# Kernel optimization log

Hardware: AMD Instinct MI355X
Metric: run time of the kernel (lower is better)

## Reference

```python
import jax, jax.numpy as jnp
import numpy as np

EPS = 0.3  # residual scaling from init_kwargs
N, E = 50000, 800000
IN_DIM, HID, OUT = 256, 64, 40


def setup_inputs() -> dict:
    key = jax.random.key(0)
    ks = jax.random.split(key, 8)
    h = jax.random.normal(ks[0], (N, IN_DIM), dtype=jnp.float32)
    src = jax.random.randint(ks[1], (E,), 0, N, dtype=jnp.int32)
    dst = jax.random.randint(ks[2], (E,), 0, N, dtype=jnp.int32)
    t1_w = jax.random.normal(ks[3], (HID, IN_DIM), dtype=jnp.float32) * 0.05
    t1_b = jnp.zeros((HID,), jnp.float32)
    gate_w1 = jax.random.normal(ks[4], (2 * HID,), dtype=jnp.float32) * 0.1
    gate_b1 = jnp.zeros((1,), jnp.float32)
    gate_w2 = jax.random.normal(ks[5], (2 * HID,), dtype=jnp.float32) * 0.1
    gate_b2 = jnp.zeros((1,), jnp.float32)
    t2_w = jax.random.normal(ks[6], (OUT, HID), dtype=jnp.float32) * 0.05
    t2_b = jnp.zeros((OUT,), jnp.float32)
    return {"h": h, "src": src, "dst": dst, "t1_w": t1_w, "t1_b": t1_b,
            "gate_w1": gate_w1, "gate_b1": gate_b1,
            "gate_w2": gate_w2, "gate_b2": gate_b2,
            "t2_w": t2_w, "t2_b": t2_b}


def _fa_layer(x, src, dst, d, gate_w, gate_b):
    # gate over concat([h_dst, h_src]) == h_dst @ w[:H] + h_src @ w[H:]
    H = x.shape[1]
    g = jnp.tanh(x[dst] @ gate_w[:H] + x[src] @ gate_w[H:] + gate_b[0])  # [E]
    e = g * d[dst] * d[src]                                              # [E]
    # message: u_mul_e('h','e') then sum onto dst
    z = jnp.zeros_like(x).at[dst].add(x[src] * e[:, None])               # [N,H]
    return z


def reference(h, src, dst, t1_w, t1_b, gate_w1, gate_b1, gate_w2, gate_b2, t2_w, t2_b):
    n = h.shape[0]
    # degree normalization d = deg^{-1/2} (in-degree, clamped to >=1)
    deg = jnp.zeros((n,), h.dtype).at[dst].add(jnp.ones_like(dst, h.dtype))
    d = jax.lax.rsqrt(jnp.maximum(deg, 1.0))
    # dropout is identity in eval mode
    x = jax.nn.relu(h @ t1_w.T + t1_b)
    raw = x
    for gw, gb in ((gate_w1, gate_b1), (gate_w2, gate_b2)):
        x = EPS * raw + _fa_layer(x, src, dst, d, gw, gb)
    logits = x @ t2_w.T + t2_b
    return jax.nn.log_softmax(logits, axis=1)
```

## Files before the change

### kernel.cpp

```cpp
#include <hip/hip_runtime.h>
#include <hip/hip_bf16.h>
#include <math.h>

#define IN_DIM 256
#define HID 64
#define OUT_DIM 40
#define EPS_RES 0.3f
#define NBUK 256
#define CAP 5120
#define EPB 2048

typedef __attribute__((ext_vector_type(8))) short short8v;
typedef __attribute__((ext_vector_type(4))) float f32x4;

__device__ __forceinline__ float tanh_fast(float u) {
    float t = __expf(2.0f * u);
    return 1.0f - 2.0f / (t + 1.0f);
}

__device__ __forceinline__ short f2bf(float f) {
    __hip_bfloat16 b = __float2bfloat16(f);
    return __builtin_bit_cast(short, b);
}

__global__ void k_wconv(const float* __restrict__ w1, const float* __restrict__ w2,
                        short* __restrict__ wpre, short* __restrict__ w2p,
                        int* __restrict__ bcur) {
    int i = blockIdx.x * blockDim.x + threadIdx.x;
    if (i < HID * IN_DIM) wpre[i] = f2bf(w1[i]);
    if (i < 48 * HID) {
        int row = i >> 6;
        w2p[i] = f2bf(row < OUT_DIM ? w2[i] : 0.f);
    }
    if (i < NBUK) bcur[i] = 0;
}

__global__ __launch_bounds__(256) void k_bscatter(
    const int* __restrict__ src, const int* __restrict__ dst,
    int* __restrict__ bcur, unsigned int* __restrict__ edges, int E) {
    __shared__ int cnt[NBUK];
    __shared__ int lcur[NBUK];
    int tid = threadIdx.x;
    cnt[tid] = 0;
    __syncthreads();
    int base = blockIdx.x * EPB;
#pragma unroll 8
    for (int k = 0; k < EPB / 256; ++k) {
        int i = base + k * 256 + tid;
        if (i < E) atomicAdd(&cnt[dst[i] >> 8], 1);
    }
    __syncthreads();
    if (cnt[tid]) lcur[tid] = tid * CAP + atomicAdd(&bcur[tid], cnt[tid]);
    __syncthreads();
#pragma unroll 8
    for (int k = 0; k < EPB / 256; ++k) {
        int i = base + k * 256 + tid;
        if (i < E) {
            int d = dst[i];
            int p = atomicAdd(&lcur[d >> 8], 1);
            edges[p] = ((unsigned int)(d & 255) << 16) | (unsigned int)src[i];
        }
    }
}

__global__ __launch_bounds__(256) void k_bfine(
    unsigned int* __restrict__ edges, const int* __restrict__ bcur,
    int* __restrict__ rowp, int* __restrict__ rowe,
    float* __restrict__ dinv, int N) {
    __shared__ unsigned int buf[CAP];
    __shared__ int lc[NBUK];
    __shared__ int sm[NBUK];
    __shared__ int lcur[NBUK];
    int tid = threadIdx.x;
    int b = blockIdx.x;
    int start = b * CAP;
    int cnt = bcur[b];
    lc[tid] = 0;
    __syncthreads();
    for (int k = tid; k < cnt; k += 256) {
        unsigned int v = edges[start + k];
        buf[k] = v;
        atomicAdd(&lc[(v >> 16) & 255], 1);
    }
    __syncthreads();
    int v = lc[tid];
    sm[tid] = v;
    __syncthreads();
    for (int off = 1; off < NBUK; off <<= 1) {
        int t = (tid >= off) ? sm[tid - off] : 0;
        __syncthreads();
        sm[tid] += t;
        __syncthreads();
    }
    int ls = sm[tid] - v;
    lcur[tid] = ls;
    int node = b * 256 + tid;
    if (node < N) {
        rowp[node] = start + ls;
        rowe[node] = start + ls + v;
        dinv[node] = rsqrtf(fmaxf((float)v, 1.0f));
    }
    __syncthreads();
    for (int k = tid; k < cnt; k += 256) {
        unsigned int pv = buf[k];
        int lo = (pv >> 16) & 255;
        int p = atomicAdd(&lcur[lo], 1);
        edges[start + p] = pv & 0xFFFFu;
    }
}

__global__ __launch_bounds__(256) void k_gemm1(
    const float* __restrict__ h, const short* __restrict__ wpre,
    const float* __restrict__ b, const float* __restrict__ gw,
    const float* __restrict__ dinv,
    float* __restrict__ out, float* __restrict__ xs0,
    float* __restrict__ gpa, float* __restrict__ gpb, int N) {
    int tid = threadIdx.x;
    int lane = tid & 63;
    int l15 = lane & 15, lhi = lane >> 4;
    int wv = __builtin_amdgcn_readfirstlane(tid >> 6);
    int base = blockIdx.x * 64 + wv * 16;

    int ra = base + l15;
    if (ra >= N) ra = N - 1;
    const float* arow = h + (size_t)ra * IN_DIM + lhi * 8;

    f32x4 acc[4] = {{0.f,0.f,0.f,0.f},{0.f,0.f,0.f,0.f},
                    {0.f,0.f,0.f,0.f},{0.f,0.f,0.f,0.f}};

#pragma unroll
    for (int ks = 0; ks < 8; ++ks) {
        const float4* ap = (const float4*)(arow + ks * 32);
        float4 a0 = ap[0], a1 = ap[1];
        short8v af;
        af[0] = f2bf(a0.x); af[1] = f2bf(a0.y);
        af[2] = f2bf(a0.z); af[3] = f2bf(a0.w);
        af[4] = f2bf(a1.x); af[5] = f2bf(a1.y);
        af[6] = f2bf(a1.z); af[7] = f2bf(a1.w);

        const short* wk = wpre + (size_t)l15 * IN_DIM + ks * 32 + lhi * 8;
#pragma unroll
        for (int t = 0; t < 4; ++t) {
            short8v bf = *(const short8v*)(wk + t * 16 * IN_DIM);
            acc[t] = __builtin_amdgcn_mfma_f32_16x16x32_bf16(af, bf, acc[t], 0, 0, 0);
        }
    }

#pragma unroll
    for (int r = 0; r < 4; ++r) {
        int grow = base + lhi * 4 + r;
        float vals[4];
        float pa = 0.f, pb = 0.f;
#pragma unroll
        for (int t = 0; t < 4; ++t) {
            int col = t * 16 + l15;
            float v = fmaxf(acc[t][r] + b[col], 0.f);
            vals[t] = v;
            pa = fmaf(v, gw[col], pa);
            pb = fmaf(v, gw[HID + col], pb);
        }
        if (grow < N) {
            float dv = dinv[grow];
            float* o  = out + (size_t)grow * HID;
            float* os = xs0 + (size_t)grow * HID;
#pragma unroll
            for (int t = 0; t < 4; ++t) {
                o[t * 16 + l15]  = vals[t];
                os[t * 16 + l15] = vals[t] * dv;
            }
        }
#pragma unroll
        for (int m = 1; m < 16; m <<= 1) {
            pa += __shfl_xor(pa, m);
            pb += __shfl_xor(pb, m);
        }
        if (l15 == 0 && grow < N) {
            gpa[grow] = pa;
            gpb[grow] = pb;
        }
    }
}

__global__ __launch_bounds__(256) void k_gather(
    const int* __restrict__ rowp, const int* __restrict__ rowe,
    const int* __restrict__ ssrc,
    const float* __restrict__ gpa, const float* __restrict__ gpb,
    const float* __restrict__ dinv, const float* __restrict__ gbias,
    const float* __restrict__ xs, const float* __restrict__ raw,
    float* __restrict__ z, int scaled,
    const float* __restrict__ gw_next, float* __restrict__ gpa_next,
    float* __restrict__ gpb_next, int N) {
    int lane = threadIdx.x & 63;
    int wv = __builtin_amdgcn_readfirstlane(threadIdx.x >> 6);
    int t = blockIdx.x * 4 + wv;
    if (t >= N) return;

    float at = gpa[t] + gbias[0];
    float dt = dinv[t];
    float acc = EPS_RES * raw[((size_t)t << 6) + lane];
    float acc2 = 0.f;
    int k0 = rowp[t];
    int end = rowe[t];

    for (int kc = k0; kc < end; kc += 64) {
        int cnt = end - kc;
        if (cnt > 64) cnt = 64;
        int idx = kc + ((lane < cnt) ? lane : 0);
        int sv = ssrc[idx];
        float ev = tanh_fast(at + gpb[sv]) * dt;
        int evi = __builtin_bit_cast(int, ev);
        int j = 0;
        for (; j + 4 <= cnt; j += 4) {
            int s0 = __builtin_amdgcn_readlane(sv, j);
            int s1 = __builtin_amdgcn_readlane(sv, j + 1);
            int s2 = __builtin_amdgcn_readlane(sv, j + 2);
            int s3 = __builtin_amdgcn_readlane(sv, j + 3);
            float e0 = __builtin_bit_cast(float, __builtin_amdgcn_readlane(evi, j));
            float e1 = __builtin_bit_cast(float, __builtin_amdgcn_readlane(evi, j + 1));
            float e2 = __builtin_bit_cast(float, __builtin_amdgcn_readlane(evi, j + 2));
            float e3 = __builtin_bit_cast(float, __builtin_amdgcn_readlane(evi, j + 3));
            float x0 = xs[((size_t)s0 << 6) + lane];
            float x1 = xs[((size_t)s1 << 6) + lane];
            float x2 = xs[((size_t)s2 << 6) + lane];
            float x3 = xs[((size_t)s3 << 6) + lane];
            acc  = fmaf(e0, x0, acc);
            acc2 = fmaf(e1, x1, acc2);
            acc  = fmaf(e2, x2, acc);
            acc2 = fmaf(e3, x3, acc2);
        }
        for (; j < cnt; ++j) {
            int s0 = __builtin_amdgcn_readlane(sv, j);
            float e0 = __builtin_bit_cast(float, __builtin_amdgcn_readlane(evi, j));
            acc = fmaf(e0, xs[((size_t)s0 << 6) + lane], acc);
        }
    }
    acc += acc2;
    z[((size_t)t << 6) + lane] = scaled ? dt * acc : acc;

    if (gw_next) {
        float pa = acc * gw_next[lane];
        float pb = acc * gw_next[HID + lane];
#pragma unroll
        for (int m = 32; m; m >>= 1) {
            pa += __shfl_xor(pa, m);
            pb += __shfl_xor(pb, m);
        }
        if (lane == 0) {
            gpa_next[t] = pa;
            gpb_next[t] = pb;
        }
    }
}

__global__ __launch_bounds__(256) void k_head(
    const float* __restrict__ x, const short* __restrict__ w2p,
    const float* __restrict__ b2, float* __restrict__ out, int N) {
    int tid = threadIdx.x;
    int lane = tid & 63;
    int l15 = lane & 15, lhi = lane >> 4;
    int wv = __builtin_amdgcn_readfirstlane(tid >> 6);
    int base = blockIdx.x * 64 + wv * 16;

    int ra = base + l15;
    if (ra >= N) ra = N - 1;
    const float* arow = x + (size_t)ra * HID + lhi * 8;

    f32x4 acc[3] = {{0.f,0.f,0.f,0.f},{0.f,0.f,0.f,0.f},{0.f,0.f,0.f,0.f}};

#pragma unroll
    for (int ks = 0; ks < 2; ++ks) {
        const float4* ap = (const float4*)(arow + ks * 32);
        float4 a0 = ap[0], a1 = ap[1];
        short8v af;
        af[0] = f2bf(a0.x); af[1] = f2bf(a0.y);
        af[2] = f2bf(a0.z); af[3] = f2bf(a0.w);
        af[4] = f2bf(a1.x); af[5] = f2bf(a1.y);
        af[6] = f2bf(a1.z); af[7] = f2bf(a1.w);

        const short* wk = w2p + (size_t)l15 * HID + ks * 32 + lhi * 8;
#pragma unroll
        for (int t = 0; t < 3; ++t) {
            short8v bf = *(const short8v*)(wk + t * 16 * HID);
            acc[t] = __builtin_amdgcn_mfma_f32_16x16x32_bf16(af, bf, acc[t], 0, 0, 0);
        }
    }

    bool has2 = (l15 < 8);
    float b0 = b2[l15];
    float b1 = b2[l15 + 16];
    float bq = has2 ? b2[l15 + 32] : 0.f;

#pragma unroll
    for (int r = 0; r < 4; ++r) {
        int grow = base + lhi * 4 + r;
        float v0 = acc[0][r] + b0;
        float v1 = acc[1][r] + b1;
        float v2 = acc[2][r] + bq;
        float m = fmaxf(fmaxf(v0, v1), has2 ? v2 : -1e30f);
#pragma unroll
        for (int mm = 1; mm < 16; mm <<= 1) m = fmaxf(m, __shfl_xor(m, mm));
        float s = expf(v0 - m) + expf(v1 - m) + (has2 ? expf(v2 - m) : 0.f);
#pragma unroll
        for (int mm = 1; mm < 16; mm <<= 1) s += __shfl_xor(s, mm);
        float lse = m + logf(s);
        if (grow < N) {
            float* o = out + (size_t)grow * OUT_DIM;
            o[l15] = v0 - lse;
            o[l15 + 16] = v1 - lse;
            if (has2) o[l15 + 32] = v2 - lse;
        }
    }
}

extern "C" void kernel_launch(void* const* d_in, const int* in_sizes, int n_in,
                              void* d_out, int out_size, void* d_ws, size_t ws_size,
                              hipStream_t stream) {
    const float* h    = (const float*)d_in[0];
    const int*   src  = (const int*)d_in[1];
    const int*   dst  = (const int*)d_in[2];
    const float* t1_w = (const float*)d_in[3];
    const float* t1_b = (const float*)d_in[4];
    const float* gw1  = (const float*)d_in[5];
    const float* gb1  = (const float*)d_in[6];
    const float* gw2  = (const float*)d_in[7];
    const float* gb2  = (const float*)d_in[8];
    const float* t2_w = (const float*)d_in[9];
    const float* t2_b = (const float*)d_in[10];
    float* out = (float*)d_out;

    const int N = in_sizes[0] / IN_DIM;
    const int E = in_sizes[1];
    const int NEB = (E + EPB - 1) / EPB;
    const int NBB = (N + 255) / 256;

    float* ws   = (float*)d_ws;
    float* raw  = ws;
    float* xs0  = raw + (size_t)N * HID;
    float* xs1  = xs0 + (size_t)N * HID;
    float* xB   = xs0;
    float* dinv = xs1 + (size_t)N * HID;
    float* gpa1 = dinv + N;
    float* gpb1 = gpa1 + N;
    float* gpa2 = gpb1 + N;
    float* gpb2 = gpa2 + N;
    short* wpre = (short*)(gpb2 + N);
    short* w2p  = wpre + HID * IN_DIM;
    int* rowp   = (int*)(w2p + 48 * HID);
    int* rowe   = rowp + N;
    int* bcur   = rowe + N;
    unsigned int* edges = (unsigned int*)(bcur + NBUK);

    const int TB = 256;

    k_wconv<<<(HID * IN_DIM + TB - 1) / TB, TB, 0, stream>>>(t1_w, t2_w, wpre, w2p, bcur);

    k_bscatter<<<NEB, TB, 0, stream>>>(src, dst, bcur, edges, E);
    k_bfine<<<NBB, TB, 0, stream>>>(edges, bcur, rowp, rowe, dinv, N);

    k_gemm1<<<(N + 63) / 64, TB, 0, stream>>>(h, wpre, t1_b, gw1, dinv,
                                              raw, xs0, gpa1, gpb1, N);

    k_gather<<<(N + 3) / 4, TB, 0, stream>>>(rowp, rowe, (const int*)edges,
                                             gpa1, gpb1, dinv, gb1,
                                             xs0, raw, xs1, 1, gw2, gpa2, gpb2, N);

    k_gather<<<(N + 3) / 4, TB, 0, stream>>>(rowp, rowe, (const int*)edges,
                                             gpa2, gpb2, dinv, gb2,
                                             xs1, raw, xB, 0, nullptr, nullptr, nullptr, N);

    k_head<<<(N + 63) / 64, TB, 0, stream>>>(xB, w2p, t2_b, out, N);
}
```

Baseline: 144.5 us.

## Store intermediate node features in bf16 to halve gather traffic

The pre-scaled node feature buffers read by the edge-gather kernels, and the final layer output fed to the head, are now stored as bf16 instead of fp32. Each gathered neighbor row shrinks from 256 to 128 bytes, cutting the random-access memory traffic that dominates the two aggregation passes. The head kernel now loads bf16 directly into the MFMA operand instead of converting from fp32. In exchange, intermediate activations lose precision. Gathers become 2-byte-per-lane loads, which may coalesce less efficiently.

```diff
diff --git a/kernel.cpp b/kernel.cpp
--- a/kernel.cpp
+++ b/kernel.cpp
@@ -21,6 +21,10 @@
 __device__ __forceinline__ short f2bf(float f) {
     __hip_bfloat16 b = __float2bfloat16(f);
     return __builtin_bit_cast(short, b);
+}
+
+__device__ __forceinline__ float bf2f(unsigned short u) {
+    return __builtin_bit_cast(float, (unsigned int)u << 16);
 }
 
 __global__ void k_wconv(const float* __restrict__ w1, const float* __restrict__ w2,
@@ -113,7 +117,7 @@
     const float* __restrict__ h, const short* __restrict__ wpre,
     const float* __restrict__ b, const float* __restrict__ gw,
     const float* __restrict__ dinv,
-    float* __restrict__ out, float* __restrict__ xs0,
+    float* __restrict__ out, short* __restrict__ xsb0,
     float* __restrict__ gpa, float* __restrict__ gpb, int N) {
     int tid = threadIdx.x;
     int lane = tid & 63;
@@ -162,11 +166,11 @@
         if (grow < N) {
             float dv = dinv[grow];
             float* o  = out + (size_t)grow * HID;
-            float* os = xs0 + (size_t)grow * HID;
+            short* os = xsb0 + (size_t)grow * HID;
 #pragma unroll
             for (int t = 0; t < 4; ++t) {
                 o[t * 16 + l15]  = vals[t];
-                os[t * 16 + l15] = vals[t] * dv;
+                os[t * 16 + l15] = f2bf(vals[t] * dv);
             }
         }
 #pragma unroll
@@ -186,8 +190,8 @@
     const int* __restrict__ ssrc,
     const float* __restrict__ gpa, const float* __restrict__ gpb,
     const float* __restrict__ dinv, const float* __restrict__ gbias,
-    const float* __restrict__ xs, const float* __restrict__ raw,
-    float* __restrict__ z, int scaled,
+    const unsigned short* __restrict__ xsb, const float* __restrict__ raw,
+    short* __restrict__ zb, int scaled,
     const float* __restrict__ gw_next, float* __restrict__ gpa_next,
     float* __restrict__ gpb_next, int N) {
     int lane = threadIdx.x & 63;
@@ -219,10 +223,10 @@
             float e1 = __builtin_bit_cast(float, __builtin_amdgcn_readlane(evi, j + 1));
             float e2 = __builtin_bit_cast(float, __builtin_amdgcn_readlane(evi, j + 2));
             float e3 = __builtin_bit_cast(float, __builtin_amdgcn_readlane(evi, j + 3));
-            float x0 = xs[((size_t)s0 << 6) + lane];
-            float x1 = xs[((size_t)s1 << 6) + lane];
-            float x2 = xs[((size_t)s2 << 6) + lane];
-            float x3 = xs[((size_t)s3 << 6) + lane];
+            float x0 = bf2f(xsb[((size_t)s0 << 6) + lane]);
+            float x1 = bf2f(xsb[((size_t)s1 << 6) + lane]);
+            float x2 = bf2f(xsb[((size_t)s2 << 6) + lane]);
+            float x3 = bf2f(xsb[((size_t)s3 << 6) + lane]);
             acc  = fmaf(e0, x0, acc);
             acc2 = fmaf(e1, x1, acc2);
             acc  = fmaf(e2, x2, acc);
@@ -231,11 +235,11 @@
         for (; j < cnt; ++j) {
             int s0 = __builtin_amdgcn_readlane(sv, j);
             float e0 = __builtin_bit_cast(float, __builtin_amdgcn_readlane(evi, j));
-            acc = fmaf(e0, xs[((size_t)s0 << 6) + lane], acc);
+            acc = fmaf(e0, bf2f(xsb[((size_t)s0 << 6) + lane]), acc);
         }
     }
     acc += acc2;
-    z[((size_t)t << 6) + lane] = scaled ? dt * acc : acc;
+    zb[((size_t)t << 6) + lane] = f2bf(scaled ? dt * acc : acc);
 
     if (gw_next) {
         float pa = acc * gw_next[lane];
@@ -253,7 +257,7 @@
 }
 
 __global__ __launch_bounds__(256) void k_head(
-    const float* __restrict__ x, const short* __restrict__ w2p,
+    const unsigned short* __restrict__ xb, const short* __restrict__ w2p,
     const float* __restrict__ b2, float* __restrict__ out, int N) {
     int tid = threadIdx.x;
     int lane = tid & 63;
@@ -263,20 +267,13 @@
 
     int ra = base + l15;
     if (ra >= N) ra = N - 1;
-    const float* arow = x + (size_t)ra * HID + lhi * 8;
+    const short* arow = (const short*)(xb + (size_t)ra * HID + lhi * 8);
 
     f32x4 acc[3] = {{0.f,0.f,0.f,0.f},{0.f,0.f,0.f,0.f},{0.f,0.f,0.f,0.f}};
 
 #pragma unroll
     for (int ks = 0; ks < 2; ++ks) {
-        const float4* ap = (const float4*)(arow + ks * 32);
-        float4 a0 = ap[0], a1 = ap[1];
-        short8v af;
-        af[0] = f2bf(a0.x); af[1] = f2bf(a0.y);
-        af[2] = f2bf(a0.z); af[3] = f2bf(a0.w);
-        af[4] = f2bf(a1.x); af[5] = f2bf(a1.y);
-        af[6] = f2bf(a1.z); af[7] = f2bf(a1.w);
-
+        short8v af = *(const short8v*)(arow + ks * 32);
         const short* wk = w2p + (size_t)l15 * HID + ks * 32 + lhi * 8;
 #pragma unroll
         for (int t = 0; t < 3; ++t) {
@@ -335,10 +332,10 @@
 
     float* ws   = (float*)d_ws;
     float* raw  = ws;
-    float* xs0  = raw + (size_t)N * HID;
-    float* xs1  = xs0 + (size_t)N * HID;
-    float* xB   = xs0;
-    float* dinv = xs1 + (size_t)N * HID;
+    short* xsb0 = (short*)(raw + (size_t)N * HID);
+    short* xsb1 = xsb0 + (size_t)N * HID;
+    short* xBb  = xsb0;
+    float* dinv = (float*)(xsb1 + (size_t)N * HID);
     float* gpa1 = dinv + N;
     float* gpb1 = gpa1 + N;
     float* gpa2 = gpb1 + N;
@@ -358,15 +355,17 @@
     k_bfine<<<NBB, TB, 0, stream>>>(edges, bcur, rowp, rowe, dinv, N);
 
     k_gemm1<<<(N + 63) / 64, TB, 0, stream>>>(h, wpre, t1_b, gw1, dinv,
-                                              raw, xs0, gpa1, gpb1, N);
+                                              raw, xsb0, gpa1, gpb1, N);
 
     k_gather<<<(N + 3) / 4, TB, 0, stream>>>(rowp, rowe, (const int*)edges,
                                              gpa1, gpb1, dinv, gb1,
-                                             xs0, raw, xs1, 1, gw2, gpa2, gpb2, N);
+                                             (const unsigned short*)xsb0, raw,
+                                             xsb1, 1, gw2, gpa2, gpb2, N);
 
     k_gather<<<(N + 3) / 4, TB, 0, stream>>>(rowp, rowe, (const int*)edges,
                                              gpa2, gpb2, dinv, gb2,
-                                             xs1, raw, xB, 0, nullptr, nullptr, nullptr, N);
-
-    k_head<<<(N + 63) / 64, TB, 0, stream>>>(xB, w2p, t2_b, out, N);
-}
+                                             (const unsigned short*)xsb1, raw,
+                                             xBb, 0, nullptr, nullptr, nullptr, N);
+
+    k_head<<<(N + 63) / 64, TB, 0, stream>>>((const unsigned short*)xBb, w2p, t2_b, out, N);
+}
```

New measurement: 133.1 us. -7.9%, faster.
